# Performance work log

Hardware: AMD Instinct MI355X
Metric: run time of the kernel (lower is better)

Reference implementation:

```python
import jax, jax.numpy as jnp
import numpy as np

NSAMPLE = 400
STEP = round(NSAMPLE / 4)  # 100


def sample_boundary(step):
    # Matches torch meshgrid(indexing='ij') behavior in sample_boundary()
    lin2 = jnp.linspace(0.0, 1.0, 2)
    lins = jnp.linspace(0.0, 1.0, step)
    a = jnp.stack(jnp.meshgrid(lin2, lins, indexing='ij'), axis=-1).reshape(-1, 2)
    b = jnp.stack(jnp.meshgrid(lins, lin2, indexing='ij'), axis=-1).reshape(-1, 2)
    return jnp.concatenate([a, b], axis=0)  # [4*step, 2]


def setup_inputs() -> dict:
    key = jax.random.key(0)
    k1, k2 = jax.random.split(key)
    pred = jax.random.uniform(k1, (64, 4), dtype=jnp.float32)        # [B,4] boxes
    fragments = jax.random.uniform(k2, (32, 64, 2), dtype=jnp.float32)  # [F,FP,2]
    boundary = sample_boundary(STEP).reshape(1, 4 * STEP, 2).astype(jnp.float32)  # [1,BP,2]
    return {"pred": pred, "fragments": fragments, "boundary": boundary}


def reference(pred, fragments, boundary):
    B = pred.shape[0]
    F, FP, _ = fragments.shape
    # box boundary sample points: [B,BP,2]
    box_wh = pred[:, 2:] - pred[:, :2]
    box_points = boundary * box_wh[:, None, :] + pred[:, None, :2]
    # fragment_outside_box: point inside box j iff all 4 line distances >= 0
    diff_lo = fragments[:, :, None, :] - pred[None, None, :, :2]   # [F,FP,B,2]
    diff_hi = pred[None, None, :, 2:] - fragments[:, :, None, :]   # [F,FP,B,2]
    inside = jnp.all(diff_lo >= 0, axis=-1) & jnp.all(diff_hi >= 0, axis=-1)  # [F,FP,B]
    f_out_box = (~inside).astype(fragments.dtype)
    # fragment_box_distance: min over BP of squared distance, [F,FP,B]
    d = fragments[:, :, None, None, :] - box_points[None, None, :, :, :]  # [F,FP,B,BP,2]
    f_b_dist = jnp.min(jnp.sum(d * d, axis=-1), axis=-1)
    loss = jnp.sum(jnp.min(f_b_dist * f_out_box, axis=-1)) / FP
    # forward: torch.mean(torch.stack([loss])) == loss
    return loss
```

## Files before the change

### kernel.cpp

```cpp
#include <hip/hip_runtime.h>

#define NBOX 64
#define BP   400
#define NPTS 2048
#define FP   64

__global__ __launch_bounds__(256) void coverage_point_kernel(
    const float* __restrict__ pred,
    const float* __restrict__ frags,
    const float* __restrict__ boundary,
    float* __restrict__ ws)
{
    const int t  = threadIdx.x;
    const int pt = blockIdx.x;

    const float px = frags[2 * pt + 0];
    const float py = frags[2 * pt + 1];

    const int b = t & 63;
    const int j = t >> 6;

    const float lox = pred[4 * b + 0];
    const float loy = pred[4 * b + 1];
    const float hix = pred[4 * b + 2];
    const float hiy = pred[4 * b + 3];
    const float whx = hix - lox;
    const float why = hiy - loy;

    const bool inside = (px >= lox) && (py >= loy) && (hix >= px) && (hiy >= py);

    const unsigned long long m = __ballot(inside);
    if (m != 0ULL) {
        if (t == 0) ws[pt] = 0.0f;
        return;
    }

    __shared__ float s_bnd[BP * 2];
    __shared__ float s_red[256];
    for (int i = t; i < BP * 2; i += 256) s_bnd[i] = boundary[i];
    __syncthreads();

    float mind = 1e30f;
    const int k0 = j * (BP / 4);
    #pragma unroll 4
    for (int k = 0; k < BP / 4; ++k) {
        const int bp = k0 + k;
        const float bx  = s_bnd[2 * bp + 0];
        const float by  = s_bnd[2 * bp + 1];
        const float bpx = bx * whx + lox;
        const float bpy = by * why + loy;
        const float dx  = px - bpx;
        const float dy  = py - bpy;
        const float d   = dx * dx + dy * dy;
        mind = fminf(mind, d);
    }

    s_red[t] = mind;
    __syncthreads();
    if (t < 64) {
        float v = fminf(fminf(s_red[t], s_red[t + 64]),
                        fminf(s_red[t + 128], s_red[t + 192]));
        #pragma unroll
        for (int off = 32; off; off >>= 1)
            v = fminf(v, __shfl_down(v, off));
        if (t == 0) ws[pt] = v;
    }
}

__global__ __launch_bounds__(256) void coverage_reduce_kernel(
    const float* __restrict__ ws, float* __restrict__ out)
{
    __shared__ float s[4];
    const int t = threadIdx.x;
    float acc = 0.0f;
    #pragma unroll
    for (int i = 0; i < NPTS / 256; ++i)
        acc += ws[t + i * 256];
    #pragma unroll
    for (int off = 32; off; off >>= 1)
        acc += __shfl_down(acc, off);
    if ((t & 63) == 0) s[t >> 6] = acc;
    __syncthreads();
    if (t == 0)
        out[0] = (s[0] + s[1] + s[2] + s[3]) * (1.0f / (float)FP);
}

extern "C" void kernel_launch(void* const* d_in, const int* in_sizes, int n_in,
                              void* d_out, int out_size, void* d_ws, size_t ws_size,
                              hipStream_t stream) {
    const float* pred     = (const float*)d_in[0];
    const float* frags    = (const float*)d_in[1];
    const float* boundary = (const float*)d_in[2];
    float* ws  = (float*)d_ws;
    float* out = (float*)d_out;

    coverage_point_kernel<<<NPTS, 256, 0, stream>>>(pred, frags, boundary, ws);
    coverage_reduce_kernel<<<1, 256, 0, stream>>>(ws, out);
}
```

Baseline: 75.33 us.

## Fuse final reduction into point kernel via atomicAdd and vectorize boundary loads

Removes the separate single-block reduction kernel: each point block now atomically adds its scaled minimum into the output, which is zeroed first with a memset. Boundary samples are loaded into shared memory as float4 and read as float2. The inner distance loop is rewritten with precomputed offsets and FMAs. This trades one kernel launch for a memset plus 2048 float atomics on a single address, and makes the summation order nondeterministic.

```diff
diff --git a/kernel.cpp b/kernel.cpp
--- a/kernel.cpp
+++ b/kernel.cpp
@@ -5,53 +5,47 @@
 #define NPTS 2048
 #define FP   64
 
-__global__ __launch_bounds__(256) void coverage_point_kernel(
+__global__ __launch_bounds__(256) void coverage_kernel(
     const float* __restrict__ pred,
     const float* __restrict__ frags,
     const float* __restrict__ boundary,
-    float* __restrict__ ws)
+    float* __restrict__ out)
 {
     const int t  = threadIdx.x;
     const int pt = blockIdx.x;
+    const int b  = t & 63;
+    const int j  = t >> 6;
 
     const float px = frags[2 * pt + 0];
     const float py = frags[2 * pt + 1];
-
-    const int b = t & 63;
-    const int j = t >> 6;
 
     const float lox = pred[4 * b + 0];
     const float loy = pred[4 * b + 1];
     const float hix = pred[4 * b + 2];
     const float hiy = pred[4 * b + 3];
+
+    const bool inside = (px >= lox) && (py >= loy) && (hix >= px) && (hiy >= py);
+    if (__ballot(inside) != 0ULL) return;
+
+    __shared__ float4 s_bnd4[BP / 2];
+    __shared__ float  s_red[256];
+    if (t < BP / 2) s_bnd4[t] = ((const float4*)boundary)[t];
+    __syncthreads();
+
     const float whx = hix - lox;
     const float why = hiy - loy;
+    const float ax  = px - lox;
+    const float ay  = py - loy;
 
-    const bool inside = (px >= lox) && (py >= loy) && (hix >= px) && (hiy >= py);
-
-    const unsigned long long m = __ballot(inside);
-    if (m != 0ULL) {
-        if (t == 0) ws[pt] = 0.0f;
-        return;
-    }
-
-    __shared__ float s_bnd[BP * 2];
-    __shared__ float s_red[256];
-    for (int i = t; i < BP * 2; i += 256) s_bnd[i] = boundary[i];
-    __syncthreads();
-
+    const float2* s_bnd = (const float2*)s_bnd4;
     float mind = 1e30f;
     const int k0 = j * (BP / 4);
-    #pragma unroll 4
+    #pragma unroll 5
     for (int k = 0; k < BP / 4; ++k) {
-        const int bp = k0 + k;
-        const float bx  = s_bnd[2 * bp + 0];
-        const float by  = s_bnd[2 * bp + 1];
-        const float bpx = bx * whx + lox;
-        const float bpy = by * why + loy;
-        const float dx  = px - bpx;
-        const float dy  = py - bpy;
-        const float d   = dx * dx + dy * dy;
+        const float2 bxy = s_bnd[k0 + k];
+        const float dx = fmaf(-whx, bxy.x, ax);
+        const float dy = fmaf(-why, bxy.y, ay);
+        const float d  = fmaf(dy, dy, dx * dx);
         mind = fminf(mind, d);
     }
 
@@ -63,26 +57,9 @@
         #pragma unroll
         for (int off = 32; off; off >>= 1)
             v = fminf(v, __shfl_down(v, off));
-        if (t == 0) ws[pt] = v;
+        if (t == 0)
+            atomicAdd(out, v * (1.0f / (float)FP));
     }
-}
-
-__global__ __launch_bounds__(256) void coverage_reduce_kernel(
-    const float* __restrict__ ws, float* __restrict__ out)
-{
-    __shared__ float s[4];
-    const int t = threadIdx.x;
-    float acc = 0.0f;
-    #pragma unroll
-    for (int i = 0; i < NPTS / 256; ++i)
-        acc += ws[t + i * 256];
-    #pragma unroll
-    for (int off = 32; off; off >>= 1)
-        acc += __shfl_down(acc, off);
-    if ((t & 63) == 0) s[t >> 6] = acc;
-    __syncthreads();
-    if (t == 0)
-        out[0] = (s[0] + s[1] + s[2] + s[3]) * (1.0f / (float)FP);
 }
 
 extern "C" void kernel_launch(void* const* d_in, const int* in_sizes, int n_in,
@@ -91,9 +68,8 @@
     const float* pred     = (const float*)d_in[0];
     const float* frags    = (const float*)d_in[1];
     const float* boundary = (const float*)d_in[2];
-    float* ws  = (float*)d_ws;
     float* out = (float*)d_out;
 
-    coverage_point_kernel<<<NPTS, 256, 0, stream>>>(pred, frags, boundary, ws);
-    coverage_reduce_kernel<<<1, 256, 0, stream>>>(ws, out);
+    hipMemsetAsync(out, 0, sizeof(float), stream);
+    coverage_kernel<<<NPTS, 256, 0, stream>>>(pred, frags, boundary, out);
 }
```

Measured after the change: 72.55 us. 3.7% less time.
